# Kernel optimization log

Measured on AMD Instinct MI355X. Metric: run time of the kernel, lower is better.

## Reference

```python
import jax, jax.numpy as jnp
import numpy as np

AUDIO_DIM = 256
VIDEO_DIM = 256
CONV_CH = 128
FUSED_DIM = 512
EPS = 1e-12


def _interp_linear(x, t_out):
    # x: [B, T_in, D]; torch F.interpolate(mode='linear', align_corners=False)
    t_in = x.shape[1]
    scale = t_in / t_out
    src = (jnp.arange(t_out, dtype=jnp.float32) + 0.5) * scale - 0.5
    src = jnp.maximum(src, 0.0)
    i0 = jnp.floor(src).astype(jnp.int32)
    i0 = jnp.minimum(i0, t_in - 1)
    i1 = jnp.minimum(i0 + 1, t_in - 1)
    w = (src - i0.astype(jnp.float32))[None, :, None]
    return x[:, i0, :] * (1.0 - w) + x[:, i1, :] * w


def _conv1d(x, w, b, pad):
    # x: [B, C, T], w: [O, I, K]
    y = jax.lax.conv_general_dilated(x, w, window_strides=(1,), padding=[(pad, pad)],
                                     dimension_numbers=('NCH', 'OIH', 'NCH'))
    return y + b[None, :, None]


def setup_inputs() -> dict:
    key = jax.random.key(0)
    ks = jax.random.split(key, 12)
    B, Ta, Tv = 16, 2048, 1024

    def xavier(k, shape):
        fan_out, fan_in = shape[0], int(np.prod(shape[1:]))
        std = float(np.sqrt(2.0 / (fan_in + fan_out)))
        return jax.random.normal(k, shape, dtype=jnp.float32) * std

    return {
        'audio_features': jax.random.normal(ks[0], (B, Ta, AUDIO_DIM), dtype=jnp.float32),
        'video_features': jax.random.normal(ks[1], (B, Tv, VIDEO_DIM), dtype=jnp.float32),
        'a3_w': xavier(ks[2], (CONV_CH, AUDIO_DIM, 3)), 'a3_b': jnp.zeros((CONV_CH,), jnp.float32),
        'a5_w': xavier(ks[3], (CONV_CH, AUDIO_DIM, 5)), 'a5_b': jnp.zeros((CONV_CH,), jnp.float32),
        'v3_w': xavier(ks[4], (CONV_CH, VIDEO_DIM, 3)), 'v3_b': jnp.zeros((CONV_CH,), jnp.float32),
        'v5_w': xavier(ks[5], (CONV_CH, VIDEO_DIM, 5)), 'v5_b': jnp.zeros((CONV_CH,), jnp.float32),
        'proj_w': xavier(ks[6], (FUSED_DIM, FUSED_DIM)), 'proj_b': jnp.zeros((FUSED_DIM,), jnp.float32),
    }


def reference(audio_features, video_features, a3_w, a3_b, a5_w, a5_b,
              v3_w, v3_b, v5_w, v5_b, proj_w, proj_b):
    Ta, Tv = audio_features.shape[1], video_features.shape[1]
    T = max((Ta + Tv) // 2, 1)
    # temporal alignment to common length T
    a = _interp_linear(audio_features, T)  # [B, T, 256]
    v = _interp_linear(video_features, T)  # [B, T, 256]

    gelu = lambda x: jax.nn.gelu(x, approximate=False)
    a_in = jnp.swapaxes(a, 1, 2)  # [B, 256, T]
    v_in = jnp.swapaxes(v, 1, 2)
    a_multi = jnp.concatenate([gelu(_conv1d(a_in, a3_w, a3_b, 1)),
                               gelu(_conv1d(a_in, a5_w, a5_b, 2))], axis=1)  # [B, 256, T]
    v_multi = jnp.concatenate([gelu(_conv1d(v_in, v3_w, v3_b, 1)),
                               gelu(_conv1d(v_in, v5_w, v5_b, 2))], axis=1)
    a_multi = jnp.swapaxes(a_multi, 1, 2)  # [B, T, 256]
    v_multi = jnp.swapaxes(v_multi, 1, 2)

    # cosine-similarity cross attention (torch F.normalize eps=1e-12)
    a_norm = a_multi / jnp.maximum(jnp.linalg.norm(a_multi, axis=-1, keepdims=True), EPS)
    v_norm = v_multi / jnp.maximum(jnp.linalg.norm(v_multi, axis=-1, keepdims=True), EPS)
    sim = jnp.einsum('btd,bsd->bts', a_norm, v_norm)  # [B, T, T]

    attn_a2v = jax.nn.softmax(sim, axis=-1)              # audio attends video
    attn_v2a = jnp.swapaxes(jax.nn.softmax(sim, axis=1), 1, 2)  # video attends audio
    a_enh = jnp.einsum('bts,bsd->btd', attn_a2v, v_multi)
    v_enh = jnp.einsum('bst,btd->bsd', jnp.swapaxes(attn_v2a, 1, 2), a_multi)
    # (equivalently v_enh = attn_v2a @ a_multi)
    v_enh = jnp.einsum('bts,bsd->btd', attn_v2a, a_multi)

    fused = jnp.concatenate([a + a_enh, v + v_enh], axis=-1)  # [B, T, 512]
    out = gelu(fused @ proj_w.T + proj_b)
    # dropout is identity in eval mode
    return out
```

## Files before the change

kernel.cpp:

```cpp
#include <hip/hip_runtime.h>
#include <math.h>

#define BATCH 16
#define TA 2048
#define TV 1024
#define TT 1536
#define DIM 256
#define FD 512

typedef unsigned short u16;
typedef unsigned int u32;
typedef short bf16x8 __attribute__((ext_vector_type(8)));
typedef float f32x4 __attribute__((ext_vector_type(4)));

__device__ __forceinline__ float bf2f(u16 u) {
  union { u32 i; float f; } v; v.i = ((u32)u) << 16; return v.f;
}
__device__ __forceinline__ u16 f2bf(float f) {
  union { float f; u32 i; } v; v.f = f;
  return (u16)((v.i + 0x7fffu + ((v.i >> 16) & 1u)) >> 16);
}
__device__ __forceinline__ float gelu_f(float x) {
  return 0.5f * x * (1.0f + erff(x * 0.70710678118654752440f));
}
__device__ __forceinline__ void async16(const u16* g, u16* l) {
  __builtin_amdgcn_global_load_lds((const __attribute__((address_space(1))) void*)g,
                                   (__attribute__((address_space(3))) void*)l, 16, 0, 0);
}

__global__ __launch_bounds__(256) void k_prep(
    const float* __restrict__ a3w, const float* __restrict__ a5w,
    const float* __restrict__ v3w, const float* __restrict__ v5w,
    const float* __restrict__ pw,
    u16* __restrict__ w3a, u16* __restrict__ w5a,
    u16* __restrict__ w3v, u16* __restrict__ w5v, u16* __restrict__ wp) {
  int idx = blockIdx.x * 256 + threadIdx.x;
  if (idx < 524288) {
    int e, ktaps;
    const float* src;
    u16* dst;
    if (idx < 98304)       { e = idx;          ktaps = 3; src = a3w; dst = w3a; }
    else if (idx < 262144) { e = idx - 98304;  ktaps = 5; src = a5w; dst = w5a; }
    else if (idx < 360448) { e = idx - 262144; ktaps = 3; src = v3w; dst = w3v; }
    else                   { e = idx - 360448; ktaps = 5; src = v5w; dst = w5v; }
    int kk = e >> 12, r = e & 4095;
    int j = r & 7, unit = r >> 3;
    int fb = unit >> 6, rem = unit & 63;
    int q = rem >> 4, colp = rem & 15;
    int o = fb * 16 + colp;
    int tap = kk >> 3;
    int c = (kk & 7) * 32 + q * 8 + j;
    dst[e] = f2bf(src[(o * 256 + c) * ktaps + tap]);
  } else if (idx < 786432) {
    int t = idx - 524288;
    wp[t] = f2bf(pw[t]);
  }
}

__global__ __launch_bounds__(256) void k_interp(const float* __restrict__ in,
                                                u16* __restrict__ out,
                                                int t_in, float scale) {
  int b = blockIdx.y;
  int i = blockIdx.x * 256 + threadIdx.x;
  int t = i >> 5, dg = i & 31;
  float src = ((float)t + 0.5f) * scale - 0.5f;
  src = fmaxf(src, 0.0f);
  int i0 = (int)floorf(src);
  if (i0 > t_in - 1) i0 = t_in - 1;
  int i1 = i0 + 1; if (i1 > t_in - 1) i1 = t_in - 1;
  float w = src - (float)i0;
  float om = 1.0f - w;
  const float4* p0 = (const float4*)(in + ((size_t)(b * t_in + i0)) * DIM + dg * 8);
  const float4* p1 = (const float4*)(in + ((size_t)(b * t_in + i1)) * DIM + dg * 8);
  float4 x0a = p0[0], x0b = p0[1], x1a = p1[0], x1b = p1[1];
  u16 r[8];
  r[0] = f2bf(x0a.x * om + x1a.x * w); r[1] = f2bf(x0a.y * om + x1a.y * w);
  r[2] = f2bf(x0a.z * om + x1a.z * w); r[3] = f2bf(x0a.w * om + x1a.w * w);
  r[4] = f2bf(x0b.x * om + x1b.x * w); r[5] = f2bf(x0b.y * om + x1b.y * w);
  r[6] = f2bf(x0b.z * om + x1b.z * w); r[7] = f2bf(x0b.w * om + x1b.w * w);
  u32 w0 = (u32)r[0] | ((u32)r[1] << 16), w1 = (u32)r[2] | ((u32)r[3] << 16);
  u32 w2 = (u32)r[4] | ((u32)r[5] << 16), w3 = (u32)r[6] | ((u32)r[7] << 16);
  *(uint4*)(out + ((size_t)(b * TT + t)) * DIM + dg * 8) = make_uint4(w0, w1, w2, w3);
}

__global__ __launch_bounds__(256) void k_zero(float* __restrict__ p, int n) {
  int i = blockIdx.x * 256 + threadIdx.x;
  if (i < n) p[i] = 0.f;
}

template <int TAPS>
__global__ __launch_bounds__(256) void k_convN(
    const u16* __restrict__ xa, const u16* __restrict__ xv,
    const u16* __restrict__ Wa, const u16* __restrict__ Wv,
    const float* __restrict__ ba, const float* __restrict__ bv,
    u16* __restrict__ outMa, u16* __restrict__ outMv,
    u16* __restrict__ outTa, u16* __restrict__ outTv,
    float* __restrict__ nsqa, float* __restrict__ nsqv) {
  constexpr int S = TAPS * 8;
  constexpr int OFF = (TAPS == 3) ? 1 : 2;
  constexpr int CHB = (TAPS == 3) ? 0 : 128;
  __shared__ __align__(16) u16 xs[68 * 264];
  __shared__ __align__(16) u16 Bs[2 * 4096];
  u16* tb = xs;
  int b = blockIdx.y, t0 = blockIdx.x * 64;
  int isv = blockIdx.z;
  const u16* xin = isv ? xv : xa;
  const u16* W   = isv ? Wv : Wa;
  const float* bias = isv ? bv : ba;
  u16* outM  = isv ? outMv : outMa;
  u16* outT  = isv ? outTv : outTa;
  float* nsq = isv ? nsqv : nsqa;
  int tid = threadIdx.x, wave = tid >> 6, lane = tid & 63;
  int col = lane & 15, quad = lane >> 4;

  for (int i = tid; i < 68 * 32; i += 256) {
    int row = i >> 5, un = i & 31;
    int t = t0 + row - 2;
    uint4 val = make_uint4(0, 0, 0, 0);
    if (t >= 0 && t < TT) val = *(const uint4*)(xin + ((size_t)(b * TT + t)) * DIM + un * 8);
    *(uint4*)(xs + row * 264 + un * 8) = val;
  }
  const u16* Wb = W + wave * 1024 + lane * 8;
  u16* BsW = Bs + wave * 1024;
  async16(Wb, BsW);
  async16(Wb + 512, BsW + 512);

  f32x4 acc[4][2];
  f32x4 zz = {0.f, 0.f, 0.f, 0.f};
#pragma unroll
  for (int rt = 0; rt < 4; rt++) { acc[rt][0] = zz; acc[rt][1] = zz; }

  const u16* afp = xs + (col + 2) * 264 + quad * 8;
  const u16* bfp = Bs + wave * 1024 + quad * 128 + col * 8;

#pragma unroll
  for (int s = 0; s < S; s++) {
    __syncthreads();
    if (s + 1 < S) {
      const u16* src = Wb + (size_t)(s + 1) * 4096;
      u16* dst = Bs + ((s + 1) & 1) * 4096 + wave * 1024;
      async16(src, dst);
      async16(src + 512, dst + 512);
    }
    int shift = (s >> 3) - OFF;
    int c0 = (s & 7) * 32;
    bf16x8 af[4];
#pragma unroll
    for (int rt = 0; rt < 4; rt++)
      af[rt] = *(const bf16x8*)(afp + (rt * 16 + shift) * 264 + c0);
    bf16x8 bf0 = *(const bf16x8*)(bfp + (s & 1) * 4096);
    bf16x8 bf1 = *(const bf16x8*)(bfp + (s & 1) * 4096 + 512);
#pragma unroll
    for (int rt = 0; rt < 4; rt++) {
      acc[rt][0] = __builtin_amdgcn_mfma_f32_16x16x32_bf16(af[rt], bf0, acc[rt][0], 0, 0, 0);
      acc[rt][1] = __builtin_amdgcn_mfma_f32_16x16x32_bf16(af[rt], bf1, acc[rt][1], 0, 0, 0);
    }
  }
  __syncthreads();

  float bia0 = bias[wave * 32 + col];
  float bia1 = bias[wave * 32 + 16 + col];
  float ss[4][4];
#pragma unroll
  for (int rt = 0; rt < 4; rt++)
#pragma unroll
    for (int r = 0; r < 4; r++) ss[rt][r] = 0.f;
#pragma unroll
  for (int rt = 0; rt < 4; rt++)
#pragma unroll
    for (int h = 0; h < 2; h++) {
      float bia = h ? bia1 : bia0;
      int chL = wave * 32 + h * 16 + col;
#pragma unroll
      for (int r = 0; r < 4; r++) {
        float g = gelu_f(acc[rt][h][r] + bia);
        ss[rt][r] += g * g;
        int trow = rt * 16 + quad * 4 + r;
        u16 gb = f2bf(g);
        tb[chL * 72 + trow] = gb;
        outM[((size_t)(b * TT + t0 + trow)) * DIM + CHB + chL] = gb;
      }
    }
#pragma unroll
  for (int rt = 0; rt < 4; rt++)
#pragma unroll
    for (int r = 0; r < 4; r++) {
      float v = ss[rt][r];
      v += __shfl_xor(v, 1, 64); v += __shfl_xor(v, 2, 64);
      v += __shfl_xor(v, 4, 64); v += __shfl_xor(v, 8, 64);
      if (col == 0)
        atomicAdd(&nsq[b * TT + t0 + rt * 16 + quad * 4 + r], v);
    }
  __syncthreads();
  {
    int ch = tid >> 1, half = tid & 1;
    uint4* dst = (uint4*)(outT + ((size_t)(b * 256 + CHB + ch)) * TT + t0 + half * 32);
#pragma unroll
    for (int i = 0; i < 4; i++)
      dst[i] = *(const uint4*)(tb + ch * 72 + half * 32 + i * 8);
  }
}

__global__ __launch_bounds__(256, 2) void k_flash(
    const u16* __restrict__ aM, const u16* __restrict__ vM,
    const u16* __restrict__ aMT, const u16* __restrict__ vMT,
    const float* __restrict__ naq, const float* __restrict__ nvq,
    const u16* __restrict__ a_itp, const u16* __restrict__ v_itp,
    u16* __restrict__ fused) {
  __shared__ __align__(16) u16 sKV[8 * 64 * 32];
  __shared__ __align__(16) u16 sKT[2 * 256 * 32];
  __shared__ __align__(16) u16 sE[2 * 32 * 64];
  __shared__ float sRv[64];
  __shared__ float sDen[2][64];

  int wgid = blockIdx.x;
  int xcd = wgid & 7, j = wgid >> 3;
  int g = xcd + 8 * (j / 24);
  int m0 = (j % 24) * 64;
  int b = g & 15, z = g >> 4;
  const u16* Q    = z ? vM : aM;
  const u16* KV   = z ? aM : vM;
  const u16* KVT  = z ? aMT : vMT;
  const float* nq = z ? nvq : naq;
  const float* nk = z ? naq : nvq;
  const u16* itp  = z ? v_itp : a_itp;
  int dstoff = z ? 256 : 0;

  int tid = threadIdx.x, w = tid >> 6, lane = tid & 63;
  int mg = w >> 1, ng = w & 1;
  int col = lane & 15, quad = lane >> 4;
  int li = lane >> 2;
  int sq = (lane & 3) ^ ((lane >> 3) & 3);

  bf16x8 qf[2][8];
  const u16* Qb = Q + ((size_t)(b * TT + m0 + mg * 32)) * DIM;
#pragma unroll
  for (int mt = 0; mt < 2; mt++)
#pragma unroll
    for (int kt = 0; kt < 8; kt++)
      qf[mt][kt] = *(const bf16x8*)(Qb + (size_t)(mt * 16 + col) * DIM + kt * 32 + quad * 8);

  float sra[2][4];
#pragma unroll
  for (int mt = 0; mt < 2; mt++)
#pragma unroll
    for (int r = 0; r < 4; r++)
      sra[mt][r] = 1.0f / fmaxf(
          sqrtf(nq[(size_t)b * TT + m0 + mg * 32 + mt * 16 + quad * 4 + r]), 1e-12f);

  f32x4 acc[2][8];
  f32x4 zz = {0.f, 0.f, 0.f, 0.f};
#pragma unroll
  for (int mt = 0; mt < 2; mt++)
#pragma unroll
    for (int dt = 0; dt < 8; dt++) acc[mt][dt] = zz;
  float den[2][4];
#pragma unroll
  for (int mt = 0; mt < 2; mt++)
#pragma unroll
    for (int r = 0; r < 4; r++) den[mt][r] = 0.f;

  const u16* KVb = KV + ((size_t)b * TT) * DIM;
  const u16* KTb = KVT + ((size_t)b * 256) * TT;

  for (int n0 = 0; n0 < TT; n0 += 64) {
    __syncthreads();
#pragma unroll
    for (int kk = 0; kk < 2; kk++) {
      int kt = w * 2 + kk;
#pragma unroll
      for (int i = 0; i < 4; i++) {
        const u16* src = KVb + (size_t)(n0 + i * 16 + li) * DIM + kt * 32 + sq * 8;
        async16(src, sKV + kt * 2048 + i * 512);
      }
    }
#pragma unroll
    for (int kn = 0; kn < 2; kn++)
#pragma unroll
      for (int i = 0; i < 4; i++) {
        const u16* src = KTb + (size_t)(w * 64 + i * 16 + li) * TT + n0 + kn * 32 + sq * 8;
        async16(src, sKT + kn * 8192 + w * 2048 + i * 512);
      }
    if (tid < 64)
      sRv[tid] = 1.0f / fmaxf(sqrtf(nk[(size_t)b * TT + n0 + tid]), 1e-12f);
    __syncthreads();

    f32x4 sc[2][2];
    sc[0][0] = zz; sc[0][1] = zz; sc[1][0] = zz; sc[1][1] = zz;
#pragma unroll
    for (int kt = 0; kt < 8; kt++)
#pragma unroll
      for (int nt = 0; nt < 2; nt++) {
        int row = ng * 32 + nt * 16 + col;
        bf16x8 bf = *(const bf16x8*)(sKV + kt * 2048 + row * 32 +
                                     ((quad ^ ((row >> 1) & 3)) << 3));
        sc[0][nt] = __builtin_amdgcn_mfma_f32_16x16x32_bf16(qf[0][kt], bf, sc[0][nt], 0, 0, 0);
        sc[1][nt] = __builtin_amdgcn_mfma_f32_16x16x32_bf16(qf[1][kt], bf, sc[1][nt], 0, 0, 0);
      }

#pragma unroll
    for (int mt = 0; mt < 2; mt++)
#pragma unroll
      for (int nt = 0; nt < 2; nt++) {
        int c = ng * 32 + nt * 16 + col;
        float rv = sRv[c];
#pragma unroll
        for (int r = 0; r < 4; r++) {
          float e = __expf(sc[mt][nt][r] * sra[mt][r] * rv);
          den[mt][r] += e;
          int row = mt * 16 + quad * 4 + r;
          sE[mg * 2048 + row * 64 + (((c >> 3) ^ ((row >> 1) & 7)) << 3) + (c & 7)] =
              f2bf(e);
        }
      }
    __syncthreads();

#pragma unroll
    for (int kn = 0; kn < 2; kn++) {
      bf16x8 ea0, ea1;
      {
        int row = col;
        ea0 = *(const bf16x8*)(sE + mg * 2048 + row * 64 +
                               (((kn * 4 + quad) ^ ((row >> 1) & 7)) << 3));
        row = 16 + col;
        ea1 = *(const bf16x8*)(sE + mg * 2048 + row * 64 +
                               (((kn * 4 + quad) ^ ((row >> 1) & 7)) << 3));
      }
#pragma unroll
      for (int dt = 0; dt < 8; dt++) {
        int drow = ng * 128 + dt * 16 + col;
        bf16x8 bf = *(const bf16x8*)(sKT + kn * 8192 + drow * 32 +
                                     ((quad ^ ((drow >> 1) & 3)) << 3));
        acc[0][dt] = __builtin_amdgcn_mfma_f32_16x16x32_bf16(ea0, bf, acc[0][dt], 0, 0, 0);
        acc[1][dt] = __builtin_amdgcn_mfma_f32_16x16x32_bf16(ea1, bf, acc[1][dt], 0, 0, 0);
      }
    }
  }

#pragma unroll
  for (int mt = 0; mt < 2; mt++)
#pragma unroll
    for (int r = 0; r < 4; r++) {
      float v = den[mt][r];
      v += __shfl_xor(v, 1, 64); v += __shfl_xor(v, 2, 64);
      v += __shfl_xor(v, 4, 64); v += __shfl_xor(v, 8, 64);
      if (col == 0) sDen[ng][mg * 32 + mt * 16 + quad * 4 + r] = v;
    }
  __syncthreads();

#pragma unroll
  for (int mt = 0; mt < 2; mt++)
#pragma unroll
    for (int r = 0; r < 4; r++) {
      int row = mg * 32 + mt * 16 + quad * 4 + r;
      int t = m0 + row;
      float dinv = 1.0f / (sDen[0][row] + sDen[1][row]);
      const u16* ip = itp + ((size_t)(b * TT + t)) * DIM;
      u16* op = fused + ((size_t)(b * TT + t)) * FD + dstoff;
#pragma unroll
      for (int dt = 0; dt < 8; dt++) {
        int d = ng * 128 + dt * 16 + col;
        float val = acc[mt][dt][r] * dinv + bf2f(ip[d]);
        op[d] = f2bf(val);
      }
    }
}

__global__ __launch_bounds__(256) void k_proj(const u16* __restrict__ Am,
                                              const u16* __restrict__ Bw,
                                              const float* __restrict__ bias,
                                              float* __restrict__ out) {
  __shared__ u16 As[128 * 32], Bs[128 * 32];
  int m0 = blockIdx.y * 128, n0 = blockIdx.x * 128;
  int tid = threadIdx.x, wave = tid >> 6, lane = tid & 63;
  int col = lane & 15, quad = lane >> 4;
  int wm = (wave >> 1) * 64, wn = (wave & 1) * 64;
  int lrow = lane >> 2, lcol = (lane & 3) * 8;
  const u16* Ab = Am + (size_t)m0 * FD;
  const u16* Bb = Bw + (size_t)n0 * FD;
  f32x4 acc[4][4];
  f32x4 zz = {0.f, 0.f, 0.f, 0.f};
#pragma unroll
  for (int i = 0; i < 4; i++)
#pragma unroll
    for (int j = 0; j < 4; j++) acc[i][j] = zz;

  for (int kt = 0; kt < 16; kt++) {
    int k0 = kt * 32;
    __syncthreads();
#pragma unroll
    for (int i = 0; i < 2; i++) {
      int rb = wave * 32 + i * 16;
      async16(Ab + ((size_t)(rb + lrow)) * FD + k0 + lcol, As + rb * 32);
      async16(Bb + ((size_t)(rb + lrow)) * FD + k0 + lcol, Bs + rb * 32);
    }
    __syncthreads();
    bf16x8 af[4], bfr[4];
#pragma unroll
    for (int mt = 0; mt < 4; mt++) af[mt] = *(const bf16x8*)(As + (wm + mt * 16 + col) * 32 + quad * 8);
#pragma unroll
    for (int nt = 0; nt < 4; nt++) bfr[nt] = *(const bf16x8*)(Bs + (wn + nt * 16 + col) * 32 + quad * 8);
#pragma unroll
    for (int mt = 0; mt < 4; mt++)
#pragma unroll
      for (int nt = 0; nt < 4; nt++)
        acc[mt][nt] = __builtin_amdgcn_mfma_f32_16x16x32_bf16(af[mt], bfr[nt], acc[mt][nt], 0, 0, 0);
  }
#pragma unroll
  for (int nt = 0; nt < 4; nt++) {
    float bia = bias[n0 + wn + nt * 16 + col];
#pragma unroll
    for (int mt = 0; mt < 4; mt++)
#pragma unroll
      for (int r = 0; r < 4; r++) {
        int row = m0 + wm + mt * 16 + quad * 4 + r;
        int cc = n0 + wn + nt * 16 + col;
        out[(size_t)row * FD + cc] = gelu_f(acc[mt][nt][r] + bia);
      }
  }
}

extern "C" void kernel_launch(void* const* d_in, const int* in_sizes, int n_in,
                              void* d_out, int out_size, void* d_ws, size_t ws_size,
                              hipStream_t stream) {
  const float* audio = (const float*)d_in[0];
  const float* video = (const float*)d_in[1];
  const float* a3w = (const float*)d_in[2];
  const float* a3b = (const float*)d_in[3];
  const float* a5w = (const float*)d_in[4];
  const float* a5b = (const float*)d_in[5];
  const float* v3w = (const float*)d_in[6];
  const float* v3b = (const float*)d_in[7];
  const float* v5w = (const float*)d_in[8];
  const float* v5b = (const float*)d_in[9];
  const float* pw  = (const float*)d_in[10];
  const float* pb  = (const float*)d_in[11];
  float* out = (float*)d_out;

  char* ws = (char*)d_ws;
  size_t off = 0;
  auto alloc = [&](size_t bytes) {
    char* p = ws + off;
    off += (bytes + 255) & ~(size_t)255;
    return p;
  };
  size_t szItp = (size_t)BATCH * TT * DIM * 2;
  u16* a_itp = (u16*)alloc(szItp);
  u16* v_itp = (u16*)alloc(szItp);
  u16* aM  = (u16*)alloc(szItp);
  u16* vM  = (u16*)alloc(szItp);
  u16* aMT = (u16*)alloc(szItp);
  u16* vMT = (u16*)alloc(szItp);
  float* naq = (float*)alloc((size_t)BATCH * TT * 4);
  float* nvq = (float*)alloc((size_t)BATCH * TT * 4);
  u16* fusedb = (u16*)alloc((size_t)BATCH * TT * FD * 2);
  u16* w3a = (u16*)alloc(3 * 128 * 256 * 2);
  u16* w5a = (u16*)alloc(5 * 128 * 256 * 2);
  u16* w3v = (u16*)alloc(3 * 128 * 256 * 2);
  u16* w5v = (u16*)alloc(5 * 128 * 256 * 2);
  u16* wp  = (u16*)alloc(512 * 512 * 2);

  k_prep<<<3072, 256, 0, stream>>>(a3w, a5w, v3w, v5w, pw, w3a, w5a, w3v, w5v, wp);
  k_interp<<<dim3(192, 16), 256, 0, stream>>>(audio, a_itp, TA, (float)((double)TA / TT));
  k_interp<<<dim3(192, 16), 256, 0, stream>>>(video, v_itp, TV, (float)((double)TV / TT));
  k_zero<<<192, 256, 0, stream>>>(naq, 2 * BATCH * TT);
  k_convN<3><<<dim3(24, 16, 2), 256, 0, stream>>>(a_itp, v_itp, w3a, w3v, a3b, v3b,
                                                  aM, vM, aMT, vMT, naq, nvq);
  k_convN<5><<<dim3(24, 16, 2), 256, 0, stream>>>(a_itp, v_itp, w5a, w5v, a5b, v5b,
                                                  aM, vM, aMT, vMT, naq, nvq);
  k_flash<<<768, 256, 0, stream>>>(aM, vM, aMT, vMT, naq, nvq, a_itp, v_itp, fusedb);
  k_proj<<<dim3(4, 192), 256, 0, stream>>>(fusedb, wp, pb, out);
}
```

Baseline: 352.9 us.

## Double-buffer K/V tiles in flash kernel with larger 192-row workgroups

The flash attention kernel now uses 768-thread workgroups covering 192 query rows, so each staged K/V tile is reused by three times as many rows. K, K-transpose and key norms are double-buffered, with the next tile's async loads issued before computing on the current one, and a lighter LDS-only barrier sits between the score and PV phases. The aim is to hide global-load latency and cut the number of K/V reloads. In exchange, LDS use per workgroup grows and the grid shrinks to 256 blocks, which may reduce occupancy and latency hiding across workgroups.

```diff
diff --git a/kernel.cpp b/kernel.cpp
--- a/kernel.cpp
+++ b/kernel.cpp
@@ -201,22 +201,23 @@
   }
 }
 
-__global__ __launch_bounds__(256, 2) void k_flash(
+__global__ __launch_bounds__(768, 3) void k_flash(
     const u16* __restrict__ aM, const u16* __restrict__ vM,
     const u16* __restrict__ aMT, const u16* __restrict__ vMT,
     const float* __restrict__ naq, const float* __restrict__ nvq,
     const u16* __restrict__ a_itp, const u16* __restrict__ v_itp,
     u16* __restrict__ fused) {
-  __shared__ __align__(16) u16 sKV[8 * 64 * 32];
-  __shared__ __align__(16) u16 sKT[2 * 256 * 32];
-  __shared__ __align__(16) u16 sE[2 * 32 * 64];
-  __shared__ float sRv[64];
-  __shared__ float sDen[2][64];
+  __shared__ __align__(16) u16 sKV[2][8 * 64 * 32];
+  __shared__ __align__(16) u16 sKT[2][2 * 256 * 32];
+  __shared__ __align__(16) u16 sE[6][32 * 64];
+  __shared__ float sQn[192];
+  __shared__ float sRvB[2][64];
+  __shared__ float sDen[2][192];
 
   int wgid = blockIdx.x;
-  int xcd = wgid & 7, j = wgid >> 3;
-  int g = xcd + 8 * (j / 24);
-  int m0 = (j % 24) * 64;
+  int xcd = wgid & 7, slot = wgid >> 3;
+  int g = xcd * 4 + (slot >> 3);
+  int m0 = (slot & 7) * 192;
   int b = g & 15, z = g >> 4;
   const u16* Q    = z ? vM : aM;
   const u16* KV   = z ? aM : vM;
@@ -232,6 +233,26 @@
   int li = lane >> 2;
   int sq = (lane & 3) ^ ((lane >> 3) & 3);
 
+  const u16* KVb = KV + ((size_t)b * TT) * DIM;
+  const u16* KTb = KVT + ((size_t)b * 256) * TT;
+
+  auto stage = [&](int cb, int n0s) {
+#pragma unroll
+    for (int it = 0; it < 6; it++) {
+      int u = w + it * 12;
+      if (u < 32) {
+        int kt = u >> 2, i = u & 3;
+        async16(KVb + (size_t)(n0s + i * 16 + li) * DIM + kt * 32 + sq * 8,
+                &sKV[cb][kt * 2048 + i * 512]);
+      } else if (u < 64) {
+        int v2 = u - 32;
+        int kn = v2 >> 4, r16 = v2 & 15;
+        async16(KTb + (size_t)(r16 * 16 + li) * TT + n0s + kn * 32 + sq * 8,
+                &sKT[cb][kn * 8192 + r16 * 512]);
+      }
+    }
+  };
+
   bf16x8 qf[2][8];
   const u16* Qb = Q + ((size_t)(b * TT + m0 + mg * 32)) * DIM;
 #pragma unroll
@@ -240,13 +261,9 @@
     for (int kt = 0; kt < 8; kt++)
       qf[mt][kt] = *(const bf16x8*)(Qb + (size_t)(mt * 16 + col) * DIM + kt * 32 + quad * 8);
 
-  float sra[2][4];
-#pragma unroll
-  for (int mt = 0; mt < 2; mt++)
-#pragma unroll
-    for (int r = 0; r < 4; r++)
-      sra[mt][r] = 1.0f / fmaxf(
-          sqrtf(nq[(size_t)b * TT + m0 + mg * 32 + mt * 16 + quad * 4 + r]), 1e-12f);
+  if (tid < 192) sQn[tid] = 1.0f / fmaxf(sqrtf(nq[(size_t)b * TT + m0 + tid]), 1e-12f);
+  if (tid < 64)  sRvB[0][tid] = 1.0f / fmaxf(sqrtf(nk[(size_t)b * TT + tid]), 1e-12f);
+  stage(0, 0);
 
   f32x4 acc[2][8];
   f32x4 zz = {0.f, 0.f, 0.f, 0.f};
@@ -260,81 +277,78 @@
 #pragma unroll
     for (int r = 0; r < 4; r++) den[mt][r] = 0.f;
 
-  const u16* KVb = KV + ((size_t)b * TT) * DIM;
-  const u16* KTb = KVT + ((size_t)b * 256) * TT;
-
-  for (int n0 = 0; n0 < TT; n0 += 64) {
-    __syncthreads();
-#pragma unroll
-    for (int kk = 0; kk < 2; kk++) {
-      int kt = w * 2 + kk;
-#pragma unroll
-      for (int i = 0; i < 4; i++) {
-        const u16* src = KVb + (size_t)(n0 + i * 16 + li) * DIM + kt * 32 + sq * 8;
-        async16(src, sKV + kt * 2048 + i * 512);
-      }
-    }
-#pragma unroll
-    for (int kn = 0; kn < 2; kn++)
-#pragma unroll
-      for (int i = 0; i < 4; i++) {
-        const u16* src = KTb + (size_t)(w * 64 + i * 16 + li) * TT + n0 + kn * 32 + sq * 8;
-        async16(src, sKT + kn * 8192 + w * 2048 + i * 512);
-      }
-    if (tid < 64)
-      sRv[tid] = 1.0f / fmaxf(sqrtf(nk[(size_t)b * TT + n0 + tid]), 1e-12f);
-    __syncthreads();
+  __syncthreads();
+
+  int cur = 0;
+  for (int t = 0; t < 24; t++) {
+    float rvn = 0.f;
+    if (t < 23) {
+      if (tid < 64) rvn = nk[(size_t)b * TT + (t + 1) * 64 + tid];
+      stage(cur ^ 1, (t + 1) * 64);
+    }
 
     f32x4 sc[2][2];
     sc[0][0] = zz; sc[0][1] = zz; sc[1][0] = zz; sc[1][1] = zz;
+    const u16* KVs = &sKV[cur][0];
 #pragma unroll
     for (int kt = 0; kt < 8; kt++)
 #pragma unroll
       for (int nt = 0; nt < 2; nt++) {
         int row = ng * 32 + nt * 16 + col;
-        bf16x8 bf = *(const bf16x8*)(sKV + kt * 2048 + row * 32 +
+        bf16x8 bf = *(const bf16x8*)(KVs + kt * 2048 + row * 32 +
                                      ((quad ^ ((row >> 1) & 3)) << 3));
         sc[0][nt] = __builtin_amdgcn_mfma_f32_16x16x32_bf16(qf[0][kt], bf, sc[0][nt], 0, 0, 0);
         sc[1][nt] = __builtin_amdgcn_mfma_f32_16x16x32_bf16(qf[1][kt], bf, sc[1][nt], 0, 0, 0);
       }
 
 #pragma unroll
-    for (int mt = 0; mt < 2; mt++)
+    for (int mt = 0; mt < 2; mt++) {
+      f32x4 srv4 = *(const f32x4*)&sQn[mg * 32 + mt * 16 + quad * 4];
 #pragma unroll
       for (int nt = 0; nt < 2; nt++) {
         int c = ng * 32 + nt * 16 + col;
-        float rv = sRv[c];
+        float rv = sRvB[cur][c];
 #pragma unroll
         for (int r = 0; r < 4; r++) {
-          float e = __expf(sc[mt][nt][r] * sra[mt][r] * rv);
+          float e = __expf(sc[mt][nt][r] * srv4[r] * rv);
           den[mt][r] += e;
           int row = mt * 16 + quad * 4 + r;
-          sE[mg * 2048 + row * 64 + (((c >> 3) ^ ((row >> 1) & 7)) << 3) + (c & 7)] =
-              f2bf(e);
+          sE[mg][row * 64 + (((c >> 3) ^ ((row >> 1) & 7)) << 3) + (c & 7)] = f2bf(e);
         }
       }
-    __syncthreads();
-
+    }
+
+    __builtin_amdgcn_sched_barrier(0);
+    asm volatile("s_waitcnt lgkmcnt(0)" ::: "memory");
+    __builtin_amdgcn_s_barrier();
+    __builtin_amdgcn_sched_barrier(0);
+
+    const u16* KTs = &sKT[cur][0];
 #pragma unroll
     for (int kn = 0; kn < 2; kn++) {
       bf16x8 ea0, ea1;
       {
         int row = col;
-        ea0 = *(const bf16x8*)(sE + mg * 2048 + row * 64 +
+        ea0 = *(const bf16x8*)(&sE[mg][0] + row * 64 +
                                (((kn * 4 + quad) ^ ((row >> 1) & 7)) << 3));
         row = 16 + col;
-        ea1 = *(const bf16x8*)(sE + mg * 2048 + row * 64 +
+        ea1 = *(const bf16x8*)(&sE[mg][0] + row * 64 +
                                (((kn * 4 + quad) ^ ((row >> 1) & 7)) << 3));
       }
 #pragma unroll
       for (int dt = 0; dt < 8; dt++) {
         int drow = ng * 128 + dt * 16 + col;
-        bf16x8 bf = *(const bf16x8*)(sKT + kn * 8192 + drow * 32 +
+        bf16x8 bf = *(const bf16x8*)(KTs + kn * 8192 + drow * 32 +
                                      ((quad ^ ((drow >> 1) & 3)) << 3));
         acc[0][dt] = __builtin_amdgcn_mfma_f32_16x16x32_bf16(ea0, bf, acc[0][dt], 0, 0, 0);
         acc[1][dt] = __builtin_amdgcn_mfma_f32_16x16x32_bf16(ea1, bf, acc[1][dt], 0, 0, 0);
       }
     }
+
+    if (t < 23 && tid < 64)
+      sRvB[cur ^ 1][tid] = 1.0f / fmaxf(sqrtf(rvn), 1e-12f);
+    __syncthreads();
+    cur ^= 1;
   }
 
 #pragma unroll
@@ -468,6 +482,6 @@
                                                   aM, vM, aMT, vMT, naq, nvq);
   k_convN<5><<<dim3(24, 16, 2), 256, 0, stream>>>(a_itp, v_itp, w5a, w5v, a5b, v5b,
                                                   aM, vM, aMT, vMT, naq, nvq);
-  k_flash<<<768, 256, 0, stream>>>(aM, vM, aMT, vMT, naq, nvq, a_itp, v_itp, fusedb);
+  k_flash<<<256, 768, 0, stream>>>(aM, vM, aMT, vMT, naq, nvq, a_itp, v_itp, fusedb);
   k_proj<<<dim3(4, 192), 256, 0, stream>>>(fusedb, wp, pb, out);
 }
```

Result: slower. 528.9 us (+49.9%).

## Overlap next-tile K/V staging with PV MFMA in flash kernel

Applied to the files above, without the earlier changes.

Restructures the flash attention loop so the next tile's K rows are prefetched asynchronously during the P·V MFMA phase, and the transposed V tile is loaded right after it. Manual s_waitcnt and s_barrier with sched_barriers replace the plain __syncthreads. The key-norm reciprocal is computed per thread from prefetched registers instead of going through shared memory. The aim is to hide global-to-LDS latency behind compute, at the cost of fragile hand-tuned waitcnt counts and extra register pressure.

```diff
diff --git a/kernel.cpp b/kernel.cpp
--- a/kernel.cpp
+++ b/kernel.cpp
@@ -210,7 +210,6 @@
   __shared__ __align__(16) u16 sKV[8 * 64 * 32];
   __shared__ __align__(16) u16 sKT[2 * 256 * 32];
   __shared__ __align__(16) u16 sE[2 * 32 * 64];
-  __shared__ float sRv[64];
   __shared__ float sDen[2][64];
 
   int wgid = blockIdx.x;
@@ -232,6 +231,29 @@
   int li = lane >> 2;
   int sq = (lane & 3) ^ ((lane >> 3) & 3);
 
+  const u16* KVb = KV + ((size_t)b * TT) * DIM;
+  const u16* KTb = KVT + ((size_t)b * 256) * TT;
+  const float* nkB = nk + (size_t)b * TT;
+
+  auto stageKV = [&](int n0s) {
+#pragma unroll
+    for (int kk = 0; kk < 2; kk++) {
+      int kt = w * 2 + kk;
+#pragma unroll
+      for (int i = 0; i < 4; i++)
+        async16(KVb + (size_t)(n0s + i * 16 + li) * DIM + kt * 32 + sq * 8,
+                sKV + kt * 2048 + i * 512);
+    }
+  };
+  auto stageKT = [&](int n0s) {
+#pragma unroll
+    for (int kn = 0; kn < 2; kn++)
+#pragma unroll
+      for (int i = 0; i < 4; i++)
+        async16(KTb + (size_t)(w * 64 + i * 16 + li) * TT + n0s + kn * 32 + sq * 8,
+                sKT + kn * 8192 + w * 2048 + i * 512);
+  };
+
   bf16x8 qf[2][8];
   const u16* Qb = Q + ((size_t)(b * TT + m0 + mg * 32)) * DIM;
 #pragma unroll
@@ -248,6 +270,9 @@
       sra[mt][r] = 1.0f / fmaxf(
           sqrtf(nq[(size_t)b * TT + m0 + mg * 32 + mt * 16 + quad * 4 + r]), 1e-12f);
 
+  int c0 = ng * 32 + col, c1 = ng * 32 + 16 + col;
+  float rvRaw0 = nkB[c0], rvRaw1 = nkB[c1];
+
   f32x4 acc[2][8];
   f32x4 zz = {0.f, 0.f, 0.f, 0.f};
 #pragma unroll
@@ -260,31 +285,12 @@
 #pragma unroll
     for (int r = 0; r < 4; r++) den[mt][r] = 0.f;
 
-  const u16* KVb = KV + ((size_t)b * TT) * DIM;
-  const u16* KTb = KVT + ((size_t)b * 256) * TT;
-
-  for (int n0 = 0; n0 < TT; n0 += 64) {
-    __syncthreads();
-#pragma unroll
-    for (int kk = 0; kk < 2; kk++) {
-      int kt = w * 2 + kk;
-#pragma unroll
-      for (int i = 0; i < 4; i++) {
-        const u16* src = KVb + (size_t)(n0 + i * 16 + li) * DIM + kt * 32 + sq * 8;
-        async16(src, sKV + kt * 2048 + i * 512);
-      }
-    }
-#pragma unroll
-    for (int kn = 0; kn < 2; kn++)
-#pragma unroll
-      for (int i = 0; i < 4; i++) {
-        const u16* src = KTb + (size_t)(w * 64 + i * 16 + li) * TT + n0 + kn * 32 + sq * 8;
-        async16(src, sKT + kn * 8192 + w * 2048 + i * 512);
-      }
-    if (tid < 64)
-      sRv[tid] = 1.0f / fmaxf(sqrtf(nk[(size_t)b * TT + n0 + tid]), 1e-12f);
-    __syncthreads();
-
+  stageKV(0);
+  stageKT(0);
+  __syncthreads();
+
+  for (int t = 0; t < 24; t++) {
+    int n0 = t * 64;
     f32x4 sc[2][2];
     sc[0][0] = zz; sc[0][1] = zz; sc[1][0] = zz; sc[1][1] = zz;
 #pragma unroll
@@ -297,13 +303,15 @@
         sc[0][nt] = __builtin_amdgcn_mfma_f32_16x16x32_bf16(qf[0][kt], bf, sc[0][nt], 0, 0, 0);
         sc[1][nt] = __builtin_amdgcn_mfma_f32_16x16x32_bf16(qf[1][kt], bf, sc[1][nt], 0, 0, 0);
       }
-
+    float rvi[2];
+    rvi[0] = 1.0f / fmaxf(sqrtf(rvRaw0), 1e-12f);
+    rvi[1] = 1.0f / fmaxf(sqrtf(rvRaw1), 1e-12f);
 #pragma unroll
     for (int mt = 0; mt < 2; mt++)
 #pragma unroll
       for (int nt = 0; nt < 2; nt++) {
         int c = ng * 32 + nt * 16 + col;
-        float rv = sRv[c];
+        float rv = rvi[nt];
 #pragma unroll
         for (int r = 0; r < 4; r++) {
           float e = __expf(sc[mt][nt][r] * sra[mt][r] * rv);
@@ -313,8 +321,15 @@
               f2bf(e);
         }
       }
-    __syncthreads();
-
+
+    __builtin_amdgcn_sched_barrier(0);
+    asm volatile("s_waitcnt vmcnt(0) lgkmcnt(0)" ::: "memory");
+    __builtin_amdgcn_s_barrier();
+    __builtin_amdgcn_sched_barrier(0);
+
+    int nn = (t < 23) ? (n0 + 64) : 0;
+    float rvA = nkB[nn + c0], rvB = nkB[nn + c1];
+    if (t < 23) stageKV(n0 + 64);
 #pragma unroll
     for (int kn = 0; kn < 2; kn++) {
       bf16x8 ea0, ea1;
@@ -335,6 +350,19 @@
         acc[1][dt] = __builtin_amdgcn_mfma_f32_16x16x32_bf16(ea1, bf, acc[1][dt], 0, 0, 0);
       }
     }
+
+    __builtin_amdgcn_sched_barrier(0);
+    asm volatile("s_waitcnt lgkmcnt(0)" ::: "memory");
+    __builtin_amdgcn_s_barrier();
+    __builtin_amdgcn_sched_barrier(0);
+
+    if (t < 23) stageKT(n0 + 64);
+    __builtin_amdgcn_sched_barrier(0);
+    asm volatile("s_waitcnt vmcnt(8) lgkmcnt(0)" ::: "memory");
+    __builtin_amdgcn_s_barrier();
+    __builtin_amdgcn_sched_barrier(0);
+
+    rvRaw0 = rvA; rvRaw1 = rvB;
   }
 
 #pragma unroll
```

Result: faster. 336.7 us (-4.6%).
